# Optimization experiments

Hardware: AMD Instinct MI355X
Metric: run time of the kernel (lower is better)

## Reference

```python
import jax, jax.numpy as jnp
import numpy as np

N_QUBITS = 10
N_GEN = 4
Q_DEPTH = 6
BATCH = 1024


def _cz_chain_diag(n):
    # Diagonal of the CZ chain CZ(0,1) CZ(1,2) ... CZ(n-2,n-1):
    # phase (-1)^(# adjacent 1-1 pairs) per computational basis state.
    idx = np.arange(2 ** n)
    bits = (idx[:, None] >> np.arange(n - 1, -1, -1)) & 1  # wire 0 = most significant (PennyLane)
    pairs = (bits[:, :-1] & bits[:, 1:]).sum(axis=1)
    return ((-1.0) ** pairs).astype(np.float32).reshape((2,) * n)

_CZ = jnp.asarray(_cz_chain_diag(N_QUBITS))


def _ry(t):
    c = jnp.cos(0.5 * t)
    s = jnp.sin(0.5 * t)
    return jnp.stack([jnp.stack([c, -s]), jnp.stack([s, c])]).astype(jnp.complex64)


def _rx(t):
    c = jnp.cos(0.5 * t).astype(jnp.complex64)
    js = (1j * jnp.sin(0.5 * t)).astype(jnp.complex64)
    return jnp.stack([jnp.stack([c, -js]), jnp.stack([-js, c])])


def _apply_1q(state, gate, wire):
    # state: (2,)*n complex statevector; apply 2x2 gate on `wire`.
    state = jnp.moveaxis(state, wire, -1)
    state = jnp.einsum('...j,ij->...i', state, gate)
    return jnp.moveaxis(state, -1, wire)


def _circuit(noise_s, weights, cz):
    # noise_s: (n_qubits,), weights: (q_depth, n_qubits)
    n = noise_s.shape[0]
    state = jnp.zeros((2,) * n, jnp.complex64).at[(0,) * n].set(1.0)
    for q in range(n):
        state = _apply_1q(state, _ry(noise_s[q]), q)
        state = _apply_1q(state, _rx(noise_s[q]), q)

    def layer(st, w):
        for q in range(n):
            st = _apply_1q(st, _ry(w[q]), q)
        return st * cz, None

    state, _ = jax.lax.scan(layer, state, weights)
    # <X_q> = Re <psi| X_q |psi>; X_q flips the q-th wire.
    return jnp.stack([jnp.real(jnp.vdot(state, jnp.flip(state, axis=q))) for q in range(n)])


def setup_inputs() -> dict:
    key = jax.random.key(0)
    k1, k2 = jax.random.split(key)
    noise = jax.random.normal(k1, (BATCH, N_QUBITS), dtype=jnp.float32)
    q_params = jax.random.uniform(k2, (N_GEN, Q_DEPTH, N_QUBITS), dtype=jnp.float32)  # q_delta=1.0 * rand
    return {"noise": noise, "q_params": q_params}


def reference(noise, q_params):
    per_sample = lambda ns, w: _circuit(ns, w, _CZ)
    per_gen = jax.vmap(lambda w: jax.vmap(lambda ns: per_sample(ns, w))(noise))(q_params)  # (G, B, n)
    out = jnp.transpose(per_gen, (1, 0, 2)).reshape(noise.shape[0], N_GEN * N_QUBITS)
    return out.astype(jnp.float32)
```

## Files before the change

### kernel.cpp

```cpp
#include <hip/hip_runtime.h>

#define NQ 10
#define NG 4
#define QD 6
#define NBATCH 1024
#define WPB 4


typedef float v2f __attribute__((ext_vector_type(2)));
typedef unsigned u2v __attribute__((ext_vector_type(2)));

template<int CTRL>
__device__ __forceinline__ float dpp1(float x) {
    return __int_as_float(__builtin_amdgcn_update_dpp(
        0, __float_as_int(x), CTRL, 0xF, 0xF, false));
}
template<int CTRL>
__device__ __forceinline__ v2f dpp2(v2f x) {
    v2f r; r.x = dpp1<CTRL>(x.x); r.y = dpp1<CTRL>(x.y); return r;
}

struct FX1 { static __device__ __forceinline__ v2f f(v2f x){ return dpp2<0xB1>(x); } };
struct FX2 { static __device__ __forceinline__ v2f f(v2f x){ return dpp2<0x4E>(x); } };
struct FX4 { static __device__ __forceinline__ v2f f(v2f x){ return dpp2<0x1B>(dpp2<0x141>(x)); } };
struct FX8 { static __device__ __forceinline__ v2f f(v2f x){ return dpp2<0x128>(x); } };
struct FX16 {
    static __device__ __forceinline__ v2f f(v2f x){
        v2f r;
        r.x = __int_as_float(__builtin_amdgcn_ds_swizzle(__float_as_int(x.x), 0x401F));
        r.y = __int_as_float(__builtin_amdgcn_ds_swizzle(__float_as_int(x.y), 0x401F));
        return r;
    }
};
struct FX32 {
    static __device__ __forceinline__ v2f f(v2f x){
        v2f r; r.x = __shfl_xor(x.x, 32, 64); r.y = __shfl_xor(x.y, 32, 64); return r;
    }
};

__device__ __forceinline__ float rlane(float v, int idx) {
    return __int_as_float(__builtin_amdgcn_readlane(__float_as_int(v), idx));
}

#if __has_builtin(__builtin_amdgcn_permlane32_swap) && __has_builtin(__builtin_amdgcn_permlane16_swap)
#define HAVE_SWAP 1
__device__ __forceinline__ void tr_b5b3(v2f (&s)[16]) {
#pragma unroll
    for (int j = 0; j < 8; ++j) {
        {
            u2v r = __builtin_amdgcn_permlane32_swap(
                __float_as_uint(s[j].x), __float_as_uint(s[j + 8].x), false, false);
            s[j].x = __uint_as_float(r.x); s[j + 8].x = __uint_as_float(r.y);
        }
        {
            u2v r = __builtin_amdgcn_permlane32_swap(
                __float_as_uint(s[j].y), __float_as_uint(s[j + 8].y), false, false);
            s[j].y = __uint_as_float(r.x); s[j + 8].y = __uint_as_float(r.y);
        }
    }
}
__device__ __forceinline__ void tr_b4b2(v2f (&s)[16]) {
#pragma unroll
    for (int jj = 0; jj < 8; ++jj) {
        const int j = (jj & 3) | ((jj >> 2) << 3);
        {
            u2v r = __builtin_amdgcn_permlane16_swap(
                __float_as_uint(s[j].x), __float_as_uint(s[j + 4].x), false, false);
            s[j].x = __uint_as_float(r.x); s[j + 4].x = __uint_as_float(r.y);
        }
        {
            u2v r = __builtin_amdgcn_permlane16_swap(
                __float_as_uint(s[j].y), __float_as_uint(s[j + 4].y), false, false);
            s[j].y = __uint_as_float(r.x); s[j + 4].y = __uint_as_float(r.y);
        }
    }
}
#else
#define HAVE_SWAP 0
#endif

__device__ __forceinline__ float wave_reduce(float x) {
    x += __int_as_float(__builtin_amdgcn_update_dpp(0, __float_as_int(x), 0x111, 0xF, 0xF, true));
    x += __int_as_float(__builtin_amdgcn_update_dpp(0, __float_as_int(x), 0x112, 0xF, 0xF, true));
    x += __int_as_float(__builtin_amdgcn_update_dpp(0, __float_as_int(x), 0x114, 0xF, 0xF, true));
    x += __int_as_float(__builtin_amdgcn_update_dpp(0, __float_as_int(x), 0x118, 0xF, 0xF, true));
    x += __int_as_float(__builtin_amdgcn_update_dpp(0, __float_as_int(x), 0x142, 0xA, 0xF, false));
    x += __int_as_float(__builtin_amdgcn_update_dpp(0, __float_as_int(x), 0x143, 0xC, 0xF, false));
    return __int_as_float(__builtin_amdgcn_readlane(__float_as_int(x), 63));
}

__device__ __forceinline__ v2f cmul(v2f a, v2f b) {
    v2f r;
    r.x = a.x * b.x - a.y * b.y;
    r.y = a.x * b.y + a.y * b.x;
    return r;
}

template<int M>
__device__ __forceinline__ void intra_rot(v2f (&s)[16], float c, float sn) {
#pragma unroll
    for (int j = 0; j < 16; ++j)
        if ((j & M) == 0) {
            const int k = j | M;
            v2f v0 = s[j], v1 = s[k];
            s[j] = v0 * c - v1 * sn;
            s[k] = v0 * sn + v1 * c;
        }
}

template<class PF, int LM>
__device__ __forceinline__ void cross_rot(v2f (&s)[16], float c, float sn, int lane) {
    const float sv = (lane & LM) ? sn : -sn;
#pragma unroll
    for (int j = 0; j < 16; ++j) {
        v2f m = s[j] * sv;
        v2f p = PF::f(m);
        s[j] = s[j] * c - p;
    }
}

template<class PF>
__device__ __forceinline__ float cross_exp(const v2f (&s)[16]) {
    v2f acc = {0.f, 0.f};
#pragma unroll
    for (int j = 0; j < 16; ++j) {
        v2f p = PF::f(s[j]);
        acc += s[j] * p;
    }
    return acc.x + acc.y;
}

template<int M>
__device__ __forceinline__ float intra_exp(const v2f (&s)[16]) {
    v2f acc = {0.f, 0.f};
#pragma unroll
    for (int j = 0; j < 16; ++j)
        acc += s[j] * s[j ^ M];
    return acc.x + acc.y;
}

__global__ __launch_bounds__(64 * WPB) void qsim_kernel(
    const float* __restrict__ noise,
    const float* __restrict__ qp,
    float* __restrict__ out)
{
    const int wave = threadIdx.x >> 6;
    const int lane = threadIdx.x & 63;
    const int g    = blockIdx.x & 3;
    const int b    = (blockIdx.x >> 2) * WPB + wave;

    float nc[NQ], ns[NQ];
#pragma unroll
    for (int q = 0; q < NQ; ++q) {
        float t = 0.5f * noise[b * NQ + q];
        __sincosf(t, &ns[q], &nc[q]);
    }

    float wcv, wsv;
    {
        const int widx = (lane < QD * NQ) ? lane : 0;
        float t = 0.5f * qp[g * (QD * NQ) + widx];
        __sincosf(t, &wsv, &wcv);
    }

    auto fac = [&](int q, int bit) -> v2f {
        float cc = nc[q], ss = ns[q];
        v2f r;
        if (bit) { r.x = cc * ss; r.y = -r.x; }
        else     { r.x = cc * cc; r.y = -ss * ss; }
        return r;
    };

    v2f h = {1.f, 0.f};
#pragma unroll
    for (int p = 4; p <= 9; ++p)
        h = cmul(h, fac(NQ - 1 - p, (lane >> (p - 4)) & 1));

    v2f s[16];
    {
        v2f t01[4], t23[4];
#pragma unroll
        for (int a = 0; a < 4; ++a) {
            t01[a] = cmul(fac(9, a & 1), fac(8, (a >> 1) & 1));
            t23[a] = cmul(fac(7, a & 1), fac(6, (a >> 1) & 1));
        }
        v2f pre[4];
#pragma unroll
        for (int a = 0; a < 4; ++a) pre[a] = cmul(h, t01[a]);
#pragma unroll
        for (int j = 0; j < 16; ++j) s[j] = cmul(pre[j & 3], t23[j >> 2]);
    }

    float czs[16];
#pragma unroll
    for (int j = 0; j < 16; ++j) {
        unsigned i = ((unsigned)lane << 4) | (unsigned)j;
        czs[j] = (__popc(i & (i >> 1)) & 1) ? -1.f : 1.f;
    }

#pragma unroll 1
    for (int l = 0; l < QD; ++l) {
        const int base = l * NQ;
        float c[NQ], sn[NQ];
#pragma unroll
        for (int q = 0; q < NQ; ++q) {
            c[q]  = rlane(wcv, base + q);
            sn[q] = rlane(wsv, base + q);
        }

        intra_rot<1>(s, c[9], sn[9]);
        intra_rot<2>(s, c[8], sn[8]);
        intra_rot<4>(s, c[7], sn[7]);
        intra_rot<8>(s, c[6], sn[6]);
        cross_rot<FX1, 1>(s, c[5], sn[5], lane);
        cross_rot<FX2, 2>(s, c[4], sn[4], lane);
        cross_rot<FX4, 4>(s, c[3], sn[3], lane);
        cross_rot<FX8, 8>(s, c[2], sn[2], lane);
#if HAVE_SWAP
        tr_b5b3(s);
        tr_b4b2(s);
        intra_rot<8>(s, c[0], sn[0]);
        intra_rot<4>(s, c[1], sn[1]);
        tr_b4b2(s);
        tr_b5b3(s);
#else
        cross_rot<FX32,32>(s, c[0], sn[0], lane);
        cross_rot<FX16,16>(s, c[1], sn[1], lane);
#endif

#pragma unroll
        for (int j = 0; j < 16; ++j) s[j] *= czs[j];
    }

    float outval = 0.f;
    {
        float e9 = wave_reduce(intra_exp<1>(s));
        float e8 = wave_reduce(intra_exp<2>(s));
        float e7 = wave_reduce(intra_exp<4>(s));
        float e6 = wave_reduce(intra_exp<8>(s));
        float e5 = wave_reduce(cross_exp<FX1>(s));
        float e4 = wave_reduce(cross_exp<FX2>(s));
        float e3 = wave_reduce(cross_exp<FX4>(s));
        float e2 = wave_reduce(cross_exp<FX8>(s));
        float e0, e1;
#if HAVE_SWAP
        tr_b5b3(s);
        tr_b4b2(s);
        e0 = wave_reduce(intra_exp<8>(s));
        e1 = wave_reduce(intra_exp<4>(s));
#else
        e0 = wave_reduce(cross_exp<FX32>(s));
        e1 = wave_reduce(cross_exp<FX16>(s));
#endif
        outval = (lane == 0) ? e0 : outval;
        outval = (lane == 1) ? e1 : outval;
        outval = (lane == 2) ? e2 : outval;
        outval = (lane == 3) ? e3 : outval;
        outval = (lane == 4) ? e4 : outval;
        outval = (lane == 5) ? e5 : outval;
        outval = (lane == 6) ? e6 : outval;
        outval = (lane == 7) ? e7 : outval;
        outval = (lane == 8) ? e8 : outval;
        outval = (lane == 9) ? e9 : outval;
    }

    if (lane < NQ)
        out[b * (NG * NQ) + g * NQ + lane] = outval;
}

extern "C" void kernel_launch(void* const* d_in, const int* in_sizes, int n_in,
                              void* d_out, int out_size, void* d_ws, size_t ws_size,
                              hipStream_t stream) {
    const float* noise = (const float*)d_in[0];
    const float* qp    = (const float*)d_in[1];
    float* out = (float*)d_out;

    const int nblocks = (NBATCH * NG) / WPB;
    qsim_kernel<<<nblocks, 64 * WPB, 0, stream>>>(noise, qp, out);
}
```

Measured before the change: 96.30 us.

## Split real and imaginary statevector parts across two waves per circuit

After the initial state is built, every gate is real (RY rotations and CZ signs), so the real and imaginary parts evolve independently. Each circuit is now simulated by two waves, one per component. The imaginary part is handed over through shared memory, and the two partial expectation values are summed through LDS at the end. CZ sign flips become XOR on the sign bit, and cross-lane rotations shuffle the raw value instead of the pre-scaled one. This doubles the number of waves and halves per-wave work and registers, at the cost of two block barriers and some LDS traffic.

After: 109.1 us. 1.13x slower.

```diff
diff --git a/kernel.cpp b/kernel.cpp
--- a/kernel.cpp
+++ b/kernel.cpp
@@ -4,38 +4,29 @@
 #define NG 4
 #define QD 6
 #define NBATCH 1024
-#define WPB 4
-
-
-typedef float v2f __attribute__((ext_vector_type(2)));
+
+
 typedef unsigned u2v __attribute__((ext_vector_type(2)));
 
+template<int CTRL, int RM, int BM, bool BC>
+__device__ __forceinline__ float dppmov(float x) {
+    return __int_as_float(__builtin_amdgcn_update_dpp(
+        0, __float_as_int(x), CTRL, RM, BM, BC));
+}
 template<int CTRL>
-__device__ __forceinline__ float dpp1(float x) {
-    return __int_as_float(__builtin_amdgcn_update_dpp(
-        0, __float_as_int(x), CTRL, 0xF, 0xF, false));
-}
-template<int CTRL>
-__device__ __forceinline__ v2f dpp2(v2f x) {
-    v2f r; r.x = dpp1<CTRL>(x.x); r.y = dpp1<CTRL>(x.y); return r;
-}
-
-struct FX1 { static __device__ __forceinline__ v2f f(v2f x){ return dpp2<0xB1>(x); } };
-struct FX2 { static __device__ __forceinline__ v2f f(v2f x){ return dpp2<0x4E>(x); } };
-struct FX4 { static __device__ __forceinline__ v2f f(v2f x){ return dpp2<0x1B>(dpp2<0x141>(x)); } };
-struct FX8 { static __device__ __forceinline__ v2f f(v2f x){ return dpp2<0x128>(x); } };
+__device__ __forceinline__ float dpp1(float x) { return dppmov<CTRL,0xF,0xF,true>(x); }
+
+struct FX1 { static __device__ __forceinline__ float f(float x){ return dpp1<0xB1>(x); } };
+struct FX2 { static __device__ __forceinline__ float f(float x){ return dpp1<0x4E>(x); } };
+struct FX4 { static __device__ __forceinline__ float f(float x){ return dpp1<0x1B>(dpp1<0x141>(x)); } };
+struct FX8 { static __device__ __forceinline__ float f(float x){ return dpp1<0x128>(x); } };
 struct FX16 {
-    static __device__ __forceinline__ v2f f(v2f x){
-        v2f r;
-        r.x = __int_as_float(__builtin_amdgcn_ds_swizzle(__float_as_int(x.x), 0x401F));
-        r.y = __int_as_float(__builtin_amdgcn_ds_swizzle(__float_as_int(x.y), 0x401F));
-        return r;
+    static __device__ __forceinline__ float f(float x){
+        return __int_as_float(__builtin_amdgcn_ds_swizzle(__float_as_int(x), 0x401F));
     }
 };
 struct FX32 {
-    static __device__ __forceinline__ v2f f(v2f x){
-        v2f r; r.x = __shfl_xor(x.x, 32, 64); r.y = __shfl_xor(x.y, 32, 64); return r;
-    }
+    static __device__ __forceinline__ float f(float x){ return __shfl_xor(x, 32, 64); }
 };
 
 __device__ __forceinline__ float rlane(float v, int idx) {
@@ -44,35 +35,23 @@
 
 #if __has_builtin(__builtin_amdgcn_permlane32_swap) && __has_builtin(__builtin_amdgcn_permlane16_swap)
 #define HAVE_SWAP 1
-__device__ __forceinline__ void tr_b5b3(v2f (&s)[16]) {
-#pragma unroll
-    for (int j = 0; j < 8; ++j) {
-        {
-            u2v r = __builtin_amdgcn_permlane32_swap(
-                __float_as_uint(s[j].x), __float_as_uint(s[j + 8].x), false, false);
-            s[j].x = __uint_as_float(r.x); s[j + 8].x = __uint_as_float(r.y);
-        }
-        {
-            u2v r = __builtin_amdgcn_permlane32_swap(
-                __float_as_uint(s[j].y), __float_as_uint(s[j + 8].y), false, false);
-            s[j].y = __uint_as_float(r.x); s[j + 8].y = __uint_as_float(r.y);
-        }
-    }
-}
-__device__ __forceinline__ void tr_b4b2(v2f (&s)[16]) {
+__device__ __forceinline__ void plswap32(float &a, float &b) {
+    u2v r = __builtin_amdgcn_permlane32_swap(__float_as_uint(a), __float_as_uint(b), false, false);
+    a = __uint_as_float(r.x); b = __uint_as_float(r.y);
+}
+__device__ __forceinline__ void plswap16(float &a, float &b) {
+    u2v r = __builtin_amdgcn_permlane16_swap(__float_as_uint(a), __float_as_uint(b), false, false);
+    a = __uint_as_float(r.x); b = __uint_as_float(r.y);
+}
+__device__ __forceinline__ void tr_b5b3(float (&s)[16]) {
+#pragma unroll
+    for (int j = 0; j < 8; ++j) plswap32(s[j], s[j + 8]);
+}
+__device__ __forceinline__ void tr_b4b2(float (&s)[16]) {
 #pragma unroll
     for (int jj = 0; jj < 8; ++jj) {
         const int j = (jj & 3) | ((jj >> 2) << 3);
-        {
-            u2v r = __builtin_amdgcn_permlane16_swap(
-                __float_as_uint(s[j].x), __float_as_uint(s[j + 4].x), false, false);
-            s[j].x = __uint_as_float(r.x); s[j + 4].x = __uint_as_float(r.y);
-        }
-        {
-            u2v r = __builtin_amdgcn_permlane16_swap(
-                __float_as_uint(s[j].y), __float_as_uint(s[j + 4].y), false, false);
-            s[j].y = __uint_as_float(r.x); s[j + 4].y = __uint_as_float(r.y);
-        }
+        plswap16(s[j], s[j + 4]);
     }
 }
 #else
@@ -80,122 +59,132 @@
 #endif
 
 __device__ __forceinline__ float wave_reduce(float x) {
-    x += __int_as_float(__builtin_amdgcn_update_dpp(0, __float_as_int(x), 0x111, 0xF, 0xF, true));
-    x += __int_as_float(__builtin_amdgcn_update_dpp(0, __float_as_int(x), 0x112, 0xF, 0xF, true));
-    x += __int_as_float(__builtin_amdgcn_update_dpp(0, __float_as_int(x), 0x114, 0xF, 0xF, true));
-    x += __int_as_float(__builtin_amdgcn_update_dpp(0, __float_as_int(x), 0x118, 0xF, 0xF, true));
-    x += __int_as_float(__builtin_amdgcn_update_dpp(0, __float_as_int(x), 0x142, 0xA, 0xF, false));
-    x += __int_as_float(__builtin_amdgcn_update_dpp(0, __float_as_int(x), 0x143, 0xC, 0xF, false));
+    x += dppmov<0x111,0xF,0xF,true >(x);
+    x += dppmov<0x112,0xF,0xF,true >(x);
+    x += dppmov<0x114,0xF,0xF,true >(x);
+    x += dppmov<0x118,0xF,0xF,true >(x);
+    x += dppmov<0x142,0xA,0xF,false>(x);
+    x += dppmov<0x143,0xC,0xF,false>(x);
     return __int_as_float(__builtin_amdgcn_readlane(__float_as_int(x), 63));
 }
 
-__device__ __forceinline__ v2f cmul(v2f a, v2f b) {
-    v2f r;
-    r.x = a.x * b.x - a.y * b.y;
-    r.y = a.x * b.y + a.y * b.x;
-    return r;
-}
-
 template<int M>
-__device__ __forceinline__ void intra_rot(v2f (&s)[16], float c, float sn) {
+__device__ __forceinline__ void intra_rot(float (&s)[16], float c, float sn) {
 #pragma unroll
     for (int j = 0; j < 16; ++j)
         if ((j & M) == 0) {
             const int k = j | M;
-            v2f v0 = s[j], v1 = s[k];
+            float v0 = s[j], v1 = s[k];
             s[j] = v0 * c - v1 * sn;
             s[k] = v0 * sn + v1 * c;
         }
 }
 
 template<class PF, int LM>
-__device__ __forceinline__ void cross_rot(v2f (&s)[16], float c, float sn, int lane) {
+__device__ __forceinline__ void cross_rot(float (&s)[16], float c, float sn, int lane) {
     const float sv = (lane & LM) ? sn : -sn;
 #pragma unroll
     for (int j = 0; j < 16; ++j) {
-        v2f m = s[j] * sv;
-        v2f p = PF::f(m);
-        s[j] = s[j] * c - p;
+        float p = PF::f(s[j]);
+        s[j] = c * s[j] + sv * p;
     }
 }
 
 template<class PF>
-__device__ __forceinline__ float cross_exp(const v2f (&s)[16]) {
-    v2f acc = {0.f, 0.f};
-#pragma unroll
-    for (int j = 0; j < 16; ++j) {
-        v2f p = PF::f(s[j]);
-        acc += s[j] * p;
-    }
-    return acc.x + acc.y;
+__device__ __forceinline__ float cross_exp(const float (&s)[16]) {
+    float a = 0.f;
+#pragma unroll
+    for (int j = 0; j < 16; ++j) a += s[j] * PF::f(s[j]);
+    return a;
 }
 
 template<int M>
-__device__ __forceinline__ float intra_exp(const v2f (&s)[16]) {
-    v2f acc = {0.f, 0.f};
-#pragma unroll
-    for (int j = 0; j < 16; ++j)
-        acc += s[j] * s[j ^ M];
-    return acc.x + acc.y;
-}
-
-__global__ __launch_bounds__(64 * WPB) void qsim_kernel(
+__device__ __forceinline__ float intra_exp(const float (&s)[16]) {
+    float a = 0.f;
+#pragma unroll
+    for (int j = 0; j < 16; ++j) a += s[j] * s[j ^ M];
+    return a;
+}
+
+__global__ __launch_bounds__(256, 8) void qsim_kernel(
     const float* __restrict__ noise,
     const float* __restrict__ qp,
     float* __restrict__ out)
 {
-    const int wave = threadIdx.x >> 6;
-    const int lane = threadIdx.x & 63;
+    __shared__ float ship[2][1024];
+    __shared__ float partlds[2][16];
+
+    const int tid  = threadIdx.x;
+    const int wave = tid >> 6;
+    const int lane = tid & 63;
+    const int pc   = wave >> 1;
+    const int comp = wave & 1;
     const int g    = blockIdx.x & 3;
-    const int b    = (blockIdx.x >> 2) * WPB + wave;
-
-    float nc[NQ], ns[NQ];
-#pragma unroll
-    for (int q = 0; q < NQ; ++q) {
-        float t = 0.5f * noise[b * NQ + q];
-        __sincosf(t, &ns[q], &nc[q]);
-    }
+    const int b    = (blockIdx.x >> 2) * 2 + pc;
 
     float wcv, wsv;
     {
         const int widx = (lane < QD * NQ) ? lane : 0;
-        float t = 0.5f * qp[g * (QD * NQ) + widx];
-        __sincosf(t, &wsv, &wcv);
-    }
-
-    auto fac = [&](int q, int bit) -> v2f {
-        float cc = nc[q], ss = ns[q];
-        v2f r;
-        if (bit) { r.x = cc * ss; r.y = -r.x; }
-        else     { r.x = cc * cc; r.y = -ss * ss; }
-        return r;
-    };
-
-    v2f h = {1.f, 0.f};
-#pragma unroll
-    for (int p = 4; p <= 9; ++p)
-        h = cmul(h, fac(NQ - 1 - p, (lane >> (p - 4)) & 1));
-
-    v2f s[16];
-    {
-        v2f t01[4], t23[4];
+        __sincosf(0.5f * qp[g * (QD * NQ) + widx], &wsv, &wcv);
+    }
+
+    float s[16];
+
+    if (comp == 0) {
+        float nc[NQ], ns[NQ];
+#pragma unroll
+        for (int q = 0; q < NQ; ++q)
+            __sincosf(0.5f * noise[b * NQ + q], &ns[q], &nc[q]);
+
+        auto facr = [&](int q, int bit) { return bit ? nc[q]*ns[q] : nc[q]*nc[q]; };
+        auto faci = [&](int q, int bit) { return bit ? -nc[q]*ns[q] : -ns[q]*ns[q]; };
+
+        float hr = 1.f, hi = 0.f;
+#pragma unroll
+        for (int p = 4; p <= 9; ++p) {
+            const int q = NQ - 1 - p, bit = (lane >> (p - 4)) & 1;
+            float fr = facr(q, bit), fi = faci(q, bit);
+            float tr = hr * fr - hi * fi;
+            float ti = hr * fi + hi * fr;
+            hr = tr; hi = ti;
+        }
+        float t01r[4], t01i[4], t23r[4], t23i[4];
 #pragma unroll
         for (int a = 0; a < 4; ++a) {
-            t01[a] = cmul(fac(9, a & 1), fac(8, (a >> 1) & 1));
-            t23[a] = cmul(fac(7, a & 1), fac(6, (a >> 1) & 1));
-        }
-        v2f pre[4];
-#pragma unroll
-        for (int a = 0; a < 4; ++a) pre[a] = cmul(h, t01[a]);
-#pragma unroll
-        for (int j = 0; j < 16; ++j) s[j] = cmul(pre[j & 3], t23[j >> 2]);
-    }
-
-    float czs[16];
+            float f9r = facr(9, a & 1), f9i = faci(9, a & 1);
+            float f8r = facr(8, (a >> 1) & 1), f8i = faci(8, (a >> 1) & 1);
+            t01r[a] = f9r * f8r - f9i * f8i;
+            t01i[a] = f9r * f8i + f9i * f8r;
+            float f7r = facr(7, a & 1), f7i = faci(7, a & 1);
+            float f6r = facr(6, (a >> 1) & 1), f6i = faci(6, (a >> 1) & 1);
+            t23r[a] = f7r * f6r - f7i * f6i;
+            t23i[a] = f7r * f6i + f7i * f6r;
+        }
+        float prer[4], prei[4];
+#pragma unroll
+        for (int a = 0; a < 4; ++a) {
+            prer[a] = hr * t01r[a] - hi * t01i[a];
+            prei[a] = hr * t01i[a] + hi * t01r[a];
+        }
+#pragma unroll
+        for (int j = 0; j < 16; ++j) {
+            float rr = prer[j & 3] * t23r[j >> 2] - prei[j & 3] * t23i[j >> 2];
+            float ii = prer[j & 3] * t23i[j >> 2] + prei[j & 3] * t23r[j >> 2];
+            s[j] = rr;
+            ship[pc][j * 64 + lane] = ii;
+        }
+    }
+    __syncthreads();
+    if (comp == 1) {
+#pragma unroll
+        for (int j = 0; j < 16; ++j) s[j] = ship[pc][j * 64 + lane];
+    }
+
+    unsigned czm[16];
 #pragma unroll
     for (int j = 0; j < 16; ++j) {
         unsigned i = ((unsigned)lane << 4) | (unsigned)j;
-        czs[j] = (__popc(i & (i >> 1)) & 1) ? -1.f : 1.f;
+        czm[j] = (unsigned)(__popc(i & (i >> 1)) & 1) << 31;
     }
 
 #pragma unroll 1
@@ -227,12 +216,12 @@
         cross_rot<FX32,32>(s, c[0], sn[0], lane);
         cross_rot<FX16,16>(s, c[1], sn[1], lane);
 #endif
-
-#pragma unroll
-        for (int j = 0; j < 16; ++j) s[j] *= czs[j];
-    }
-
-    float outval = 0.f;
+#pragma unroll
+        for (int j = 0; j < 16; ++j)
+            s[j] = __uint_as_float(__float_as_uint(s[j]) ^ czm[j]);
+    }
+
+    float myp = 0.f;
     {
         float e9 = wave_reduce(intra_exp<1>(s));
         float e8 = wave_reduce(intra_exp<2>(s));
@@ -252,20 +241,22 @@
         e0 = wave_reduce(cross_exp<FX32>(s));
         e1 = wave_reduce(cross_exp<FX16>(s));
 #endif
-        outval = (lane == 0) ? e0 : outval;
-        outval = (lane == 1) ? e1 : outval;
-        outval = (lane == 2) ? e2 : outval;
-        outval = (lane == 3) ? e3 : outval;
-        outval = (lane == 4) ? e4 : outval;
-        outval = (lane == 5) ? e5 : outval;
-        outval = (lane == 6) ? e6 : outval;
-        outval = (lane == 7) ? e7 : outval;
-        outval = (lane == 8) ? e8 : outval;
-        outval = (lane == 9) ? e9 : outval;
-    }
-
-    if (lane < NQ)
-        out[b * (NG * NQ) + g * NQ + lane] = outval;
+        myp = (lane == 0) ? e0 : myp;
+        myp = (lane == 1) ? e1 : myp;
+        myp = (lane == 2) ? e2 : myp;
+        myp = (lane == 3) ? e3 : myp;
+        myp = (lane == 4) ? e4 : myp;
+        myp = (lane == 5) ? e5 : myp;
+        myp = (lane == 6) ? e6 : myp;
+        myp = (lane == 7) ? e7 : myp;
+        myp = (lane == 8) ? e8 : myp;
+        myp = (lane == 9) ? e9 : myp;
+    }
+
+    if (comp == 0 && lane < NQ) partlds[pc][lane] = myp;
+    __syncthreads();
+    if (comp == 1 && lane < NQ)
+        out[b * (NG * NQ) + g * NQ + lane] = myp + partlds[pc][lane];
 }
 
 extern "C" void kernel_launch(void* const* d_in, const int* in_sizes, int n_in,
@@ -275,6 +266,6 @@
     const float* qp    = (const float*)d_in[1];
     float* out = (float*)d_out;
 
-    const int nblocks = (NBATCH * NG) / WPB;
-    qsim_kernel<<<nblocks, 64 * WPB, 0, stream>>>(noise, qp, out);
-}
+    const int nblocks = (NBATCH * NG) / 2;
+    qsim_kernel<<<nblocks, 256, 0, stream>>>(noise, qp, out);
+}
```
